# Optimization experiments

Hardware: AMD Instinct MI355X
Metric: run time of the kernel (lower is better)

The kernel has to match this reference:

```python
import jax, jax.numpy as jnp
import numpy as np

# column-index constants for the node feature matrix and edge attributes
VM, VA, PG, QG, PD, QD = 0, 1, 2, 3, 4, 5
G_COL, B_COL = 0, 1

N_NODES = 100000
N_EDGES = 3200000
N_FEAT = 6


def setup_inputs() -> dict:
    key = jax.random.key(0)
    k1, k2, k3, k4, k5, k6 = jax.random.split(key, 6)
    pred = jax.random.normal(k1, (N_NODES, N_FEAT), dtype=jnp.float32)
    target = jax.random.normal(k2, (N_NODES, N_FEAT), dtype=jnp.float32)
    src = jax.random.randint(k3, (N_EDGES,), 0, N_NODES, dtype=jnp.int32)
    dst = jax.random.randint(k4, (N_EDGES,), 0, N_NODES, dtype=jnp.int32)
    edge_index = jnp.stack([src, dst], axis=0)
    edge_attr = jax.random.normal(k5, (N_EDGES, 2), dtype=jnp.float32)
    mask = jax.random.bernoulli(k6, 0.5, (N_NODES, N_FEAT))
    return {"pred": pred, "target": target, "edge_index": edge_index,
            "edge_attr": edge_attr, "mask": mask}


def reference(pred, target, edge_index, edge_attr, mask):
    # temp_pred[~mask] = target[~mask]
    tp = jnp.where(mask, pred, target)

    V_m = tp[:, VM]
    V_a = tp[:, VA]
    V = V_m * jnp.exp(1j * V_a)           # complex64 [N]
    V_conj = jnp.conj(V)

    # conj(Y_bus) entries on edges: G - jB
    Y_conj = edge_attr[:, G_COL] - 1j * edge_attr[:, B_COL]  # complex64 [E]

    row, col = edge_index[0], edge_index[1]
    # (Y_bus_conj @ V_conj)[i] = sum over edges (i,j) of conj(Y_ij) * conj(V_j)
    msg = Y_conj * V_conj[col]                               # gather-multiply [E]
    matvec = jax.ops.segment_sum(msg, row, num_segments=tp.shape[0])  # scatter-add [N]

    S_injection = V * matvec                                  # diag(V) @ (...)

    net_P = tp[:, PG] - tp[:, PD]
    net_Q = tp[:, QG] - tp[:, QD]
    diff = (net_P + 1j * net_Q) - S_injection

    loss = jnp.mean(jnp.abs(diff))
    real_loss = jnp.mean(jnp.abs(jnp.real(diff)))
    imag_loss = jnp.mean(jnp.abs(jnp.imag(diff)))
    return (loss, real_loss, imag_loss)
```

## Files before the change

kernel.cpp:

```cpp
#include <hip/hip_runtime.h>
#include <hip/hip_fp16.h>
#include <math.h>

constexpr int N_NODES = 100000;
constexpr int N_EDGES = 3200000;
constexpr int NF      = 6;

constexpr int BSHIFT  = 10;
constexpr int BNODES  = 1 << BSHIFT;
constexpr int NB      = (N_NODES + BNODES - 1) >> BSHIFT;
constexpr int CAP     = 33792;
constexpr int NSLICE  = 16;
constexpr int TILE    = 2048;
constexpr int EPT     = TILE / 256;
constexpr int NBLK_PART = (N_EDGES + TILE - 1) / TILE;
constexpr int VPREP_BLOCKS = (N_NODES + 255) / 256;

constexpr size_t OFF_V    = 0;
constexpr size_t OFF_REC  = OFF_V  + (size_t)N_NODES * 8;
constexpr size_t OFF_PART = OFF_REC + (size_t)NB * CAP * 8;
constexpr size_t OFF_CNT  = OFF_PART + (size_t)NB * NSLICE * BNODES * 8;
constexpr size_t WS_NEED  = OFF_CNT + 1024;

union F2U { float2 f; unsigned long long u; };

__device__ __forceinline__ float2 half2u_to_f2(unsigned u) {
    __half2 h;
    *reinterpret_cast<unsigned*>(&h) = u;
    return __half22float2(h);
}

__global__ __launch_bounds__(256) void partition_edges(
        const int* __restrict__ row, const int* __restrict__ col,
        const float2* __restrict__ attr,
        const float* __restrict__ pred, const float* __restrict__ target,
        const unsigned char* __restrict__ mask,
        float2* __restrict__ v_out,
        unsigned int* __restrict__ gcur,
        uint2* __restrict__ rec_g) {
    __shared__ unsigned int h[4][NB];
    __shared__ unsigned int cur[4][NB];
    __shared__ int wb[4][NB];
    __shared__ int dbase[NB];
    __shared__ unsigned int tot_s[NB];
    __shared__ uint2 rec_s[TILE];
    __shared__ unsigned char bkt_s[TILE];
    __shared__ int total_s;

    const int tid = threadIdx.x;
    const int w = tid >> 6;
    const int e0 = blockIdx.x * TILE;
    const int e_base = e0 + tid * EPT;
    const bool ok = e_base < N_EDGES;

    if (blockIdx.x < VPREP_BLOCKS) {
        int i = blockIdx.x * 256 + tid;
        if (i < N_NODES) {
            const int bb = i * NF;
            float vm = mask[bb + 0] ? pred[bb + 0] : target[bb + 0];
            float va = mask[bb + 1] ? pred[bb + 1] : target[bb + 1];
            float sn, cs;
            sincosf(va, &sn, &cs);
            v_out[i] = make_float2(vm * cs, vm * sn);
        }
    }

    for (int i = tid; i < 4 * NB; i += 256) {
        (&h[0][0])[i] = 0u;
        (&cur[0][0])[i] = 0u;
    }
    __syncthreads();

    int r[EPT];
    if (ok) {
        int4 ra = *(const int4*)(row + e_base);
        int4 rb = *(const int4*)(row + e_base + 4);
        r[0]=ra.x; r[1]=ra.y; r[2]=ra.z; r[3]=ra.w;
        r[4]=rb.x; r[5]=rb.y; r[6]=rb.z; r[7]=rb.w;
        #pragma unroll
        for (int k = 0; k < EPT; ++k)
            atomicAdd(&h[w][r[k] >> BSHIFT], 1u);
    }
    __syncthreads();

    if (tid < NB)
        tot_s[tid] = h[0][tid] + h[1][tid] + h[2][tid] + h[3][tid];
    __syncthreads();

    if (tid < NB) {
        int lbase = 0;
        for (int j = 0; j < tid; ++j) lbase += (int)tot_s[j];
        unsigned t0 = h[0][tid], t1 = h[1][tid], t2 = h[2][tid];
        unsigned tot = tot_s[tid];
        unsigned g = tot ? atomicAdd(&gcur[tid], tot) : 0u;
        dbase[tid] = (int)g - lbase;
        wb[0][tid] = lbase;
        wb[1][tid] = lbase + (int)t0;
        wb[2][tid] = lbase + (int)(t0 + t1);
        wb[3][tid] = lbase + (int)(t0 + t1 + t2);
        if (tid == NB - 1) total_s = lbase + (int)tot;
    }
    __syncthreads();

    if (ok) {
        int4 ca = *(const int4*)(col + e_base);
        int4 cb = *(const int4*)(col + e_base + 4);
        int c[EPT] = {ca.x, ca.y, ca.z, ca.w, cb.x, cb.y, cb.z, cb.w};
        float4 a0 = *(const float4*)(attr + e_base);
        float4 a1 = *(const float4*)(attr + e_base + 2);
        float4 a2 = *(const float4*)(attr + e_base + 4);
        float4 a3 = *(const float4*)(attr + e_base + 6);
        float gx[EPT] = {a0.x, a0.z, a1.x, a1.z, a2.x, a2.z, a3.x, a3.z};
        float gy[EPT] = {a0.y, a0.w, a1.y, a1.w, a2.y, a2.w, a3.y, a3.w};
        #pragma unroll
        for (int k = 0; k < EPT; ++k) {
            int rr = r[k];
            int b = rr >> BSHIFT;
            int slot = wb[w][b] + (int)atomicAdd(&cur[w][b], 1u);
            __half2 hh = __floats2half2_rn(gx[k], gy[k]);
            rec_s[slot] = make_uint2(
                (unsigned)c[k] | ((unsigned)(rr & (BNODES - 1)) << 17),
                *reinterpret_cast<unsigned int*>(&hh));
            bkt_s[slot] = (unsigned char)b;
        }
    }
    __syncthreads();

    const int total = total_s;
    for (int j = tid; j < total; j += 256) {
        int b = (int)bkt_s[j];
        int g = dbase[b] + j;
        if (g < CAP)
            rec_g[(size_t)b * CAP + g] = rec_s[j];
    }
}

__global__ __launch_bounds__(256) void accum_finalize(
        const unsigned int* __restrict__ gcur,
        const uint2* __restrict__ rec,
        unsigned long long* __restrict__ partials,
        unsigned int* __restrict__ sdone,
        float* __restrict__ sums,
        unsigned int* __restrict__ done_all,
        const float* __restrict__ pred,
        const float* __restrict__ target,
        const unsigned char* __restrict__ mask,
        const float2* __restrict__ v,
        float* __restrict__ out) {
    __shared__ float acc_re[BNODES];
    __shared__ float acc_im[BNODES];
    __shared__ unsigned int old_s;
    const int tid = threadIdx.x;
    const int b = blockIdx.x / NSLICE;
    const int s = blockIdx.x % NSLICE;
    int cnt = (int)min(gcur[b], (unsigned)CAP);
    for (int i = tid; i < BNODES; i += 256) { acc_re[i] = 0.f; acc_im[i] = 0.f; }
    __syncthreads();
    int per = (((cnt + NSLICE - 1) / NSLICE) + 3) & ~3;
    int st = s * per;
    int en = min(st + per, cnt);
    const uint2* rp = rec + (size_t)b * CAP;
    int j = st + 4 * tid;
    for (; j + 3 < en; j += 1024) {
        uint4 q0 = *(const uint4*)(rp + j);
        uint4 q1 = *(const uint4*)(rp + j + 2);
        int c0 = (int)(q0.x & 0x1FFFFu), li0 = (int)(q0.x >> 17);
        int c1 = (int)(q0.z & 0x1FFFFu), li1 = (int)(q0.z >> 17);
        int c2 = (int)(q1.x & 0x1FFFFu), li2 = (int)(q1.x >> 17);
        int c3 = (int)(q1.z & 0x1FFFFu), li3 = (int)(q1.z >> 17);
        float2 vv0 = v[c0];
        float2 vv1 = v[c1];
        float2 vv2 = v[c2];
        float2 vv3 = v[c3];
        float2 gb0 = half2u_to_f2(q0.y);
        float2 gb1 = half2u_to_f2(q0.w);
        float2 gb2 = half2u_to_f2(q1.y);
        float2 gb3 = half2u_to_f2(q1.w);
        atomicAdd(&acc_re[li0], fmaf(gb0.x, vv0.x, -gb0.y * vv0.y));
        atomicAdd(&acc_im[li0], -fmaf(gb0.x, vv0.y, gb0.y * vv0.x));
        atomicAdd(&acc_re[li1], fmaf(gb1.x, vv1.x, -gb1.y * vv1.y));
        atomicAdd(&acc_im[li1], -fmaf(gb1.x, vv1.y, gb1.y * vv1.x));
        atomicAdd(&acc_re[li2], fmaf(gb2.x, vv2.x, -gb2.y * vv2.y));
        atomicAdd(&acc_im[li2], -fmaf(gb2.x, vv2.y, gb2.y * vv2.x));
        atomicAdd(&acc_re[li3], fmaf(gb3.x, vv3.x, -gb3.y * vv3.y));
        atomicAdd(&acc_im[li3], -fmaf(gb3.x, vv3.y, gb3.y * vv3.x));
    }
    for (; j < en; ++j) {
        uint2 q = rp[j];
        int c0 = (int)(q.x & 0x1FFFFu), li0 = (int)(q.x >> 17);
        float2 vv0 = v[c0];
        float2 gb0 = half2u_to_f2(q.y);
        atomicAdd(&acc_re[li0], fmaf(gb0.x, vv0.x, -gb0.y * vv0.y));
        atomicAdd(&acc_im[li0], -fmaf(gb0.x, vv0.y, gb0.y * vv0.x));
    }
    __syncthreads();
    unsigned long long* p = partials + ((size_t)b * NSLICE + s) * BNODES;
    for (int i = tid; i < BNODES; i += 256) {
        F2U cvt;
        cvt.f = make_float2(acc_re[i], acc_im[i]);
        __hip_atomic_store(&p[i], cvt.u, __ATOMIC_RELAXED, __HIP_MEMORY_SCOPE_AGENT);
    }
    asm volatile("s_waitcnt vmcnt(0)" ::: "memory");
    __syncthreads();
    if (tid == 0)
        old_s = __hip_atomic_fetch_add(&sdone[b], 1u, __ATOMIC_RELAXED,
                                       __HIP_MEMORY_SCOPE_AGENT);
    __syncthreads();
    if (old_s != (unsigned)(NSLICE - 1)) return;

    const unsigned long long* pb = partials + (size_t)b * NSLICE * BNODES;
    float a = 0.f, ar = 0.f, ai = 0.f;
    for (int li = tid; li < BNODES; li += 256) {
        int i = (b << BSHIFT) + li;
        if (i >= N_NODES) break;
        float mr = 0.f, mi = 0.f;
        #pragma unroll
        for (int s2 = 0; s2 < NSLICE; ++s2) {
            F2U cvt;
            cvt.u = __hip_atomic_load(&pb[(size_t)s2 * BNODES + li],
                                      __ATOMIC_RELAXED, __HIP_MEMORY_SCOPE_AGENT);
            mr += cvt.f.x; mi += cvt.f.y;
        }
        const int bb = i * NF;
        float pg = mask[bb + 2] ? pred[bb + 2] : target[bb + 2];
        float qg = mask[bb + 3] ? pred[bb + 3] : target[bb + 3];
        float pd = mask[bb + 4] ? pred[bb + 4] : target[bb + 4];
        float qd = mask[bb + 5] ? pred[bb + 5] : target[bb + 5];
        float netP = pg - pd;
        float netQ = qg - qd;
        float2 vv = v[i];
        float s_re = vv.x * mr - vv.y * mi;
        float s_im = vv.x * mi + vv.y * mr;
        float dre = netP - s_re;
        float dim = netQ - s_im;
        ar += fabsf(dre);
        ai += fabsf(dim);
        a  += sqrtf(dre * dre + dim * dim);
    }
    #pragma unroll
    for (int off = 32; off > 0; off >>= 1) {
        a  += __shfl_down(a,  off, 64);
        ar += __shfl_down(ar, off, 64);
        ai += __shfl_down(ai, off, 64);
    }
    __shared__ float red[3][4];
    int wave = tid >> 6;
    int lane = tid & 63;
    if (lane == 0) { red[0][wave] = a; red[1][wave] = ar; red[2][wave] = ai; }
    __syncthreads();
    if (tid == 0) {
        float r0 = atomicAdd(&sums[0], red[0][0] + red[0][1] + red[0][2] + red[0][3]);
        float r1 = atomicAdd(&sums[1], red[1][0] + red[1][1] + red[1][2] + red[1][3]);
        float r2 = atomicAdd(&sums[2], red[2][0] + red[2][1] + red[2][2] + red[2][3]);
        float chk = r0 + r1 + r2;
        if (chk == chk) {
            unsigned fin = atomicAdd(done_all, 1u);
            if (fin == (unsigned)(NB - 1)) {
                const float inv = 1.0f / (float)N_NODES;
                float t0 = atomicAdd(&sums[0], 0.f);
                float t1 = atomicAdd(&sums[1], 0.f);
                float t2 = atomicAdd(&sums[2], 0.f);
                __hip_atomic_store(&out[0], t0 * inv, __ATOMIC_RELAXED, __HIP_MEMORY_SCOPE_AGENT);
                __hip_atomic_store(&out[1], t1 * inv, __ATOMIC_RELAXED, __HIP_MEMORY_SCOPE_AGENT);
                __hip_atomic_store(&out[2], t2 * inv, __ATOMIC_RELAXED, __HIP_MEMORY_SCOPE_AGENT);
            }
        }
    }
}

__global__ void node_prep_fb(const float* __restrict__ pred,
                             const float* __restrict__ target,
                             const unsigned char* __restrict__ mask,
                             float2* __restrict__ v) {
    int i = blockIdx.x * blockDim.x + threadIdx.x;
    if (i >= N_NODES) return;
    const int b = i * NF;
    float vm = mask[b + 0] ? pred[b + 0] : target[b + 0];
    float va = mask[b + 1] ? pred[b + 1] : target[b + 1];
    float s, c;
    sincosf(va, &s, &c);
    v[i] = make_float2(vm * c, vm * s);
}

__global__ void edge_scatter_fb(const int* __restrict__ row,
                                const int* __restrict__ col,
                                const float2* __restrict__ attr,
                                const float2* __restrict__ v,
                                float2* __restrict__ mv) {
    int e = blockIdx.x * blockDim.x + threadIdx.x;
    if (e >= N_EDGES) return;
    int r = row[e];
    int c = col[e];
    float2 gb = attr[e];
    float2 vv = v[c];
    float mre = fmaf(gb.x, vv.x, -gb.y * vv.y);
    float mim = -fmaf(gb.x, vv.y, gb.y * vv.x);
    atomicAdd(&mv[r].x, mre);
    atomicAdd(&mv[r].y, mim);
}

__global__ void finalize_fb(const float* __restrict__ pred,
                            const float* __restrict__ target,
                            const unsigned char* __restrict__ mask,
                            const float2* __restrict__ v,
                            const float2* __restrict__ mv,
                            float* __restrict__ sums) {
    int i = blockIdx.x * blockDim.x + threadIdx.x;
    float a = 0.f, ar = 0.f, ai = 0.f;
    if (i < N_NODES) {
        const int b = i * NF;
        float pg = mask[b + 2] ? pred[b + 2] : target[b + 2];
        float qg = mask[b + 3] ? pred[b + 3] : target[b + 3];
        float pd = mask[b + 4] ? pred[b + 4] : target[b + 4];
        float qd = mask[b + 5] ? pred[b + 5] : target[b + 5];
        float netP = pg - pd;
        float netQ = qg - qd;
        float2 vv = v[i];
        float2 m = mv[i];
        float s_re = vv.x * m.x - vv.y * m.y;
        float s_im = vv.x * m.y + vv.y * m.x;
        float dre = netP - s_re;
        float dim = netQ - s_im;
        ar = fabsf(dre);
        ai = fabsf(dim);
        a  = sqrtf(dre * dre + dim * dim);
    }
    #pragma unroll
    for (int off = 32; off > 0; off >>= 1) {
        a  += __shfl_down(a,  off, 64);
        ar += __shfl_down(ar, off, 64);
        ai += __shfl_down(ai, off, 64);
    }
    __shared__ float red[3][4];
    int wave = threadIdx.x >> 6;
    int lane = threadIdx.x & 63;
    if (lane == 0) { red[0][wave] = a; red[1][wave] = ar; red[2][wave] = ai; }
    __syncthreads();
    if (threadIdx.x == 0) {
        atomicAdd(&sums[0], red[0][0] + red[0][1] + red[0][2] + red[0][3]);
        atomicAdd(&sums[1], red[1][0] + red[1][1] + red[1][2] + red[1][3]);
        atomicAdd(&sums[2], red[2][0] + red[2][1] + red[2][2] + red[2][3]);
    }
}

__global__ void write_out_fb(const float* __restrict__ sums, float* __restrict__ out) {
    if (threadIdx.x == 0 && blockIdx.x == 0) {
        const float inv = 1.0f / (float)N_NODES;
        out[0] = sums[0] * inv;
        out[1] = sums[1] * inv;
        out[2] = sums[2] * inv;
    }
}

extern "C" void kernel_launch(void* const* d_in, const int* in_sizes, int n_in,
                              void* d_out, int out_size, void* d_ws, size_t ws_size,
                              hipStream_t stream) {
    const float*         pred   = (const float*)d_in[0];
    const float*         target = (const float*)d_in[1];
    const int*           eidx   = (const int*)d_in[2];
    const float2*        attr   = (const float2*)d_in[3];
    const unsigned char* mask   = (const unsigned char*)d_in[4];
    float* out = (float*)d_out;

    const int* row = eidx;
    const int* col = eidx + N_EDGES;

    char* ws = (char*)d_ws;
    const int B = 256;

    if (ws_size >= WS_NEED) {
        float2*             v        = (float2*)(ws + OFF_V);
        uint2*              rec_g    = (uint2*)(ws + OFF_REC);
        unsigned long long* partials = (unsigned long long*)(ws + OFF_PART);
        unsigned int*       gcur     = (unsigned int*)(ws + OFF_CNT);
        unsigned int*       sdone    = (unsigned int*)(ws + OFF_CNT + 512);
        float*              sums     = (float*)(ws + OFF_CNT + 912);
        unsigned int*       done_all = (unsigned int*)(ws + OFF_CNT + 928);

        hipMemsetAsync(ws + OFF_CNT, 0, 1024, stream);
        partition_edges<<<NBLK_PART, B, 0, stream>>>(row, col, attr,
                                                     pred, target, mask, v,
                                                     gcur, rec_g);
        accum_finalize<<<NB * NSLICE, B, 0, stream>>>(gcur, rec_g, partials,
                                                      sdone, sums, done_all,
                                                      pred, target, mask, v, out);
    } else {
        float2* v    = (float2*)ws;
        float2* mv   = (float2*)(ws + (size_t)N_NODES * 8);
        float*  sums = (float*)(ws + 2ull * N_NODES * 8);
        hipMemsetAsync(mv, 0, (size_t)N_NODES * 8 + 16, stream);
        node_prep_fb<<<(N_NODES + B - 1) / B, B, 0, stream>>>(pred, target, mask, v);
        edge_scatter_fb<<<(N_EDGES + B - 1) / B, B, 0, stream>>>(row, col, attr, v, mv);
        finalize_fb<<<(N_NODES + B - 1) / B, B, 0, stream>>>(pred, target, mask, v, mv, sums);
        write_out_fb<<<1, 64, 0, stream>>>(sums, out);
    }
}
```

Measured before the change: 186.2 us.

## Process each bucket in one 1024-thread block instead of 16 slices

The accumulation kernel drops the 16-way slicing of each node bucket and the cross-block partial-sum buffer with its completion counter. Each bucket is now handled by a single 1024-thread block that accumulates in shared memory and finalizes its nodes directly, with vectorized loads of the mask, pred and target columns. This removes the global partial writes, the reloads and the per-bucket synchronization. The cost is far fewer blocks: 98 blocks of 1024 threads instead of 1568 of 256, which leaves many CUs idle and lengthens each block's serial gather loop.

Result: slower. 221.9 us (+19.2%).

```diff
diff --git a/kernel.cpp b/kernel.cpp
--- a/kernel.cpp
+++ b/kernel.cpp
@@ -10,19 +10,15 @@
 constexpr int BNODES  = 1 << BSHIFT;
 constexpr int NB      = (N_NODES + BNODES - 1) >> BSHIFT;
 constexpr int CAP     = 33792;
-constexpr int NSLICE  = 16;
 constexpr int TILE    = 2048;
 constexpr int EPT     = TILE / 256;
 constexpr int NBLK_PART = (N_EDGES + TILE - 1) / TILE;
 constexpr int VPREP_BLOCKS = (N_NODES + 255) / 256;
 
 constexpr size_t OFF_V    = 0;
-constexpr size_t OFF_REC  = OFF_V  + (size_t)N_NODES * 8;
-constexpr size_t OFF_PART = OFF_REC + (size_t)NB * CAP * 8;
-constexpr size_t OFF_CNT  = OFF_PART + (size_t)NB * NSLICE * BNODES * 8;
+constexpr size_t OFF_REC  = OFF_V + (size_t)N_NODES * 8;
+constexpr size_t OFF_CNT  = OFF_REC + (size_t)NB * CAP * 8;
 constexpr size_t WS_NEED  = OFF_CNT + 1024;
-
-union F2U { float2 f; unsigned long long u; };
 
 __device__ __forceinline__ float2 half2u_to_f2(unsigned u) {
     __half2 h;
@@ -135,33 +131,27 @@
     }
 }
 
-__global__ __launch_bounds__(256) void accum_finalize(
+__global__ __launch_bounds__(1024) void accum_bucket(
         const unsigned int* __restrict__ gcur,
         const uint2* __restrict__ rec,
-        unsigned long long* __restrict__ partials,
-        unsigned int* __restrict__ sdone,
-        float* __restrict__ sums,
-        unsigned int* __restrict__ done_all,
+        const float2* __restrict__ v,
         const float* __restrict__ pred,
         const float* __restrict__ target,
         const unsigned char* __restrict__ mask,
-        const float2* __restrict__ v,
+        float* __restrict__ sums,
+        unsigned int* __restrict__ done_all,
         float* __restrict__ out) {
     __shared__ float acc_re[BNODES];
     __shared__ float acc_im[BNODES];
-    __shared__ unsigned int old_s;
     const int tid = threadIdx.x;
-    const int b = blockIdx.x / NSLICE;
-    const int s = blockIdx.x % NSLICE;
-    int cnt = (int)min(gcur[b], (unsigned)CAP);
-    for (int i = tid; i < BNODES; i += 256) { acc_re[i] = 0.f; acc_im[i] = 0.f; }
-    __syncthreads();
-    int per = (((cnt + NSLICE - 1) / NSLICE) + 3) & ~3;
-    int st = s * per;
-    int en = min(st + per, cnt);
+    const int b = blockIdx.x;
+    const int cnt = (int)min(gcur[b], (unsigned)CAP);
+    acc_re[tid] = 0.f;
+    acc_im[tid] = 0.f;
+    __syncthreads();
     const uint2* rp = rec + (size_t)b * CAP;
-    int j = st + 4 * tid;
-    for (; j + 3 < en; j += 1024) {
+    int j = 4 * tid;
+    for (; j + 3 < cnt; j += 4 * BNODES) {
         uint4 q0 = *(const uint4*)(rp + j);
         uint4 q1 = *(const uint4*)(rp + j + 2);
         int c0 = (int)(q0.x & 0x1FFFFu), li0 = (int)(q0.x >> 17);
@@ -185,7 +175,7 @@
         atomicAdd(&acc_re[li3], fmaf(gb3.x, vv3.x, -gb3.y * vv3.y));
         atomicAdd(&acc_im[li3], -fmaf(gb3.x, vv3.y, gb3.y * vv3.x));
     }
-    for (; j < en; ++j) {
+    for (; j < cnt; ++j) {
         uint2 q = rp[j];
         int c0 = (int)(q.x & 0x1FFFFu), li0 = (int)(q.x >> 17);
         float2 vv0 = v[c0];
@@ -194,48 +184,33 @@
         atomicAdd(&acc_im[li0], -fmaf(gb0.x, vv0.y, gb0.y * vv0.x));
     }
     __syncthreads();
-    unsigned long long* p = partials + ((size_t)b * NSLICE + s) * BNODES;
-    for (int i = tid; i < BNODES; i += 256) {
-        F2U cvt;
-        cvt.f = make_float2(acc_re[i], acc_im[i]);
-        __hip_atomic_store(&p[i], cvt.u, __ATOMIC_RELAXED, __HIP_MEMORY_SCOPE_AGENT);
-    }
-    asm volatile("s_waitcnt vmcnt(0)" ::: "memory");
-    __syncthreads();
-    if (tid == 0)
-        old_s = __hip_atomic_fetch_add(&sdone[b], 1u, __ATOMIC_RELAXED,
-                                       __HIP_MEMORY_SCOPE_AGENT);
-    __syncthreads();
-    if (old_s != (unsigned)(NSLICE - 1)) return;
-
-    const unsigned long long* pb = partials + (size_t)b * NSLICE * BNODES;
+
     float a = 0.f, ar = 0.f, ai = 0.f;
-    for (int li = tid; li < BNODES; li += 256) {
-        int i = (b << BSHIFT) + li;
-        if (i >= N_NODES) break;
-        float mr = 0.f, mi = 0.f;
-        #pragma unroll
-        for (int s2 = 0; s2 < NSLICE; ++s2) {
-            F2U cvt;
-            cvt.u = __hip_atomic_load(&pb[(size_t)s2 * BNODES + li],
-                                      __ATOMIC_RELAXED, __HIP_MEMORY_SCOPE_AGENT);
-            mr += cvt.f.x; mi += cvt.f.y;
+    {
+        int i = (b << BSHIFT) + tid;
+        if (i < N_NODES) {
+            float mr = acc_re[tid];
+            float mi = acc_im[tid];
+            const int bb = i * NF;
+            uchar2 m23 = *(const uchar2*)(mask + bb + 2);
+            uchar2 m45 = *(const uchar2*)(mask + bb + 4);
+            float2 p23 = *(const float2*)(pred + bb + 2);
+            float2 p45 = *(const float2*)(pred + bb + 4);
+            float2 t23 = *(const float2*)(target + bb + 2);
+            float2 t45 = *(const float2*)(target + bb + 4);
+            float pg = m23.x ? p23.x : t23.x;
+            float qg = m23.y ? p23.y : t23.y;
+            float pd = m45.x ? p45.x : t45.x;
+            float qd = m45.y ? p45.y : t45.y;
+            float2 vv = v[i];
+            float s_re = vv.x * mr - vv.y * mi;
+            float s_im = vv.x * mi + vv.y * mr;
+            float dre = (pg - pd) - s_re;
+            float dim = (qg - qd) - s_im;
+            ar = fabsf(dre);
+            ai = fabsf(dim);
+            a  = sqrtf(dre * dre + dim * dim);
         }
-        const int bb = i * NF;
-        float pg = mask[bb + 2] ? pred[bb + 2] : target[bb + 2];
-        float qg = mask[bb + 3] ? pred[bb + 3] : target[bb + 3];
-        float pd = mask[bb + 4] ? pred[bb + 4] : target[bb + 4];
-        float qd = mask[bb + 5] ? pred[bb + 5] : target[bb + 5];
-        float netP = pg - pd;
-        float netQ = qg - qd;
-        float2 vv = v[i];
-        float s_re = vv.x * mr - vv.y * mi;
-        float s_im = vv.x * mi + vv.y * mr;
-        float dre = netP - s_re;
-        float dim = netQ - s_im;
-        ar += fabsf(dre);
-        ai += fabsf(dim);
-        a  += sqrtf(dre * dre + dim * dim);
     }
     #pragma unroll
     for (int off = 32; off > 0; off >>= 1) {
@@ -243,15 +218,18 @@
         ar += __shfl_down(ar, off, 64);
         ai += __shfl_down(ai, off, 64);
     }
-    __shared__ float red[3][4];
+    __shared__ float red[3][16];
     int wave = tid >> 6;
     int lane = tid & 63;
     if (lane == 0) { red[0][wave] = a; red[1][wave] = ar; red[2][wave] = ai; }
     __syncthreads();
     if (tid == 0) {
-        float r0 = atomicAdd(&sums[0], red[0][0] + red[0][1] + red[0][2] + red[0][3]);
-        float r1 = atomicAdd(&sums[1], red[1][0] + red[1][1] + red[1][2] + red[1][3]);
-        float r2 = atomicAdd(&sums[2], red[2][0] + red[2][1] + red[2][2] + red[2][3]);
+        float s0 = 0.f, s1 = 0.f, s2 = 0.f;
+        #pragma unroll
+        for (int k = 0; k < 16; ++k) { s0 += red[0][k]; s1 += red[1][k]; s2 += red[2][k]; }
+        float r0 = atomicAdd(&sums[0], s0);
+        float r1 = atomicAdd(&sums[1], s1);
+        float r2 = atomicAdd(&sums[2], s2);
         float chk = r0 + r1 + r2;
         if (chk == chk) {
             unsigned fin = atomicAdd(done_all, 1u);
@@ -369,21 +347,19 @@
     const int B = 256;
 
     if (ws_size >= WS_NEED) {
-        float2*             v        = (float2*)(ws + OFF_V);
-        uint2*              rec_g    = (uint2*)(ws + OFF_REC);
-        unsigned long long* partials = (unsigned long long*)(ws + OFF_PART);
-        unsigned int*       gcur     = (unsigned int*)(ws + OFF_CNT);
-        unsigned int*       sdone    = (unsigned int*)(ws + OFF_CNT + 512);
-        float*              sums     = (float*)(ws + OFF_CNT + 912);
-        unsigned int*       done_all = (unsigned int*)(ws + OFF_CNT + 928);
+        float2*       v        = (float2*)(ws + OFF_V);
+        uint2*        rec_g    = (uint2*)(ws + OFF_REC);
+        unsigned int* gcur     = (unsigned int*)(ws + OFF_CNT);
+        float*        sums     = (float*)(ws + OFF_CNT + 912);
+        unsigned int* done_all = (unsigned int*)(ws + OFF_CNT + 928);
 
         hipMemsetAsync(ws + OFF_CNT, 0, 1024, stream);
         partition_edges<<<NBLK_PART, B, 0, stream>>>(row, col, attr,
                                                      pred, target, mask, v,
                                                      gcur, rec_g);
-        accum_finalize<<<NB * NSLICE, B, 0, stream>>>(gcur, rec_g, partials,
-                                                      sdone, sums, done_all,
-                                                      pred, target, mask, v, out);
+        accum_bucket<<<NB, BNODES, 0, stream>>>(gcur, rec_g, v,
+                                                pred, target, mask,
+                                                sums, done_all, out);
     } else {
         float2* v    = (float2*)ws;
         float2* mv   = (float2*)(ws + (size_t)N_NODES * 8);
```
